# Performance work log

Measured on AMD Instinct MI355X. Metric: run time of the kernel, lower is better.

Reference implementation:

```python
import jax, jax.numpy as jnp
import numpy as np
from jax import lax

CHAR_EMB = 30      # char_embedding_dim
N_FILT = 30        # num_cnn_filter (depthwise multiplier)
KSIZE = 3          # char_kernel_size
WORD_EMB = 100     # word_embedding_dim
MAX_WLEN = 40      # max_word_len
N_CHARS = 102      # characters.id + 2
VOCAB = 400002     # GloVe 400k + unk + pad


def setup_inputs() -> dict:
    key = jax.random.key(0)
    k1, k2, k3, k4, k5, k6 = jax.random.split(key, 6)
    B, S = 64, 128
    char_ids = jax.random.randint(k1, (B, S, MAX_WLEN), 0, N_CHARS)
    word_ids = jax.random.randint(k2, (B, S), 0, VOCAB)
    bound = (3.0 / CHAR_EMB) ** 0.5
    char_emb = jax.random.uniform(k3, (N_CHARS, CHAR_EMB), minval=-bound, maxval=bound, dtype=jnp.float32)
    # grouped Conv1d: out=CHAR_EMB*N_FILT=900, in_per_group=1, kernel=3 (OIH layout)
    fan = 1 * KSIZE + N_FILT * KSIZE
    xav = (6.0 / fan) ** 0.5
    conv_w = jax.random.uniform(k4, (CHAR_EMB * N_FILT, 1, KSIZE), minval=-xav, maxval=xav, dtype=jnp.float32)
    conv_b = jnp.zeros((CHAR_EMB * N_FILT,), dtype=jnp.float32)
    glove = jax.random.normal(k5, (VOCAB, WORD_EMB), dtype=jnp.float32)
    return {"char_ids": char_ids, "word_ids": word_ids, "char_emb": char_emb,
            "conv_w": conv_w, "conv_b": conv_b, "glove": glove}


def reference(char_ids, word_ids, char_emb, conv_w, conv_b, glove):
    B, S, W = char_ids.shape
    # char embedding lookup: [B,S,W,E] -> NCH layout [B*S, E, W]
    x = char_emb[char_ids]                       # [B,S,W,30]
    x = jnp.transpose(x, (0, 1, 3, 2)).reshape(B * S, CHAR_EMB, W)
    # depthwise (grouped) conv, groups=30, multiplier=30 -> 900 out channels, length W-K+1
    y = lax.conv_general_dilated(
        x, conv_w, window_strides=(1,), padding="VALID",
        dimension_numbers=("NCH", "OIH", "NCH"),
        feature_group_count=CHAR_EMB)            # [B*S, 900, 38]
    y = y + conv_b[None, :, None]
    pooled = jnp.max(y, axis=2).reshape(B, S, CHAR_EMB * N_FILT)  # max-over-time
    glove_e = glove[word_ids]                    # [B,S,100]
    return jnp.concatenate([pooled, glove_e], axis=2)  # [B,S,1000]
```

## Files before the change

### kernel.cpp

```cpp
#include <hip/hip_runtime.h>

#define CHAR_EMB 30
#define NFILT    30
#define WLEN     40
#define TOUT     38
#define OUTC     900
#define WORD_EMB 100
#define RP2      42

typedef float f32x2 __attribute__((ext_vector_type(2)));
typedef float f32x4 __attribute__((ext_vector_type(4)));

__device__ __forceinline__ f32x2 pk_fma(f32x2 a, f32x2 b, f32x2 c) {
    f32x2 d;
    asm("v_pk_fma_f32 %0, %1, %2, %3" : "=v"(d) : "v"(a), "v"(b), "v"(c));
    return d;
}
__device__ __forceinline__ f32x2 pk_mul(f32x2 a, f32x2 b) {
    f32x2 d;
    asm("v_pk_mul_f32 %0, %1, %2" : "=v"(d) : "v"(a), "v"(b));
    return d;
}
__device__ __forceinline__ float max3f(float a, float b, float c) {
    float d;
    asm("v_max3_f32 %0, %1, %2, %3" : "=v"(d) : "v"(a), "v"(b), "v"(c));
    return d;
}

__global__ __launch_bounds__(256, 8) void encoder_kernel(
    const int*   __restrict__ char_ids,
    const int*   __restrict__ word_ids,
    const float* __restrict__ char_emb,
    const float* __restrict__ conv_w,
    const float* __restrict__ conv_b,
    const float* __restrict__ glove,
    float*       __restrict__ out,
    int BS)
{
    const int nA   = 2 * blockIdx.x;
    const int nB   = nA + 1;
    const bool hasB = (nB < BS);
    const int tid  = threadIdx.x;

    __shared__ int cid[2 * WLEN];
    __shared__ __align__(16) f32x2 xs[CHAR_EMB * RP2];

    float* orowA = out + (long)nA * (OUTC + WORD_EMB);
    float* orowB = out + (long)nB * (OUTC + WORD_EMB);

    if (tid < 2 * WLEN) {
        cid[tid] = (tid < WLEN || hasB) ? char_ids[nA * WLEN + tid] : 0;
    }
    __syncthreads();

    for (int i = tid; i < WLEN * (CHAR_EMB / 2); i += 256) {
        const int t  = i / (CHAR_EMB / 2);
        const int cp = i - t * (CHAR_EMB / 2);
        const int c  = 2 * cp;
        const f32x2 a = *reinterpret_cast<const f32x2*>(char_emb + cid[t] * CHAR_EMB + c);
        const f32x2 b = *reinterpret_cast<const f32x2*>(char_emb + cid[WLEN + t] * CHAR_EMB + c);
        f32x2 v0; v0.x = a.x; v0.y = b.x;
        f32x2 v1; v1.x = a.y; v1.y = b.y;
        xs[(c    ) * RP2 + t] = v0;
        xs[(c + 1) * RP2 + t] = v1;
    }
    __syncthreads();

    if (tid < 240) {
        const int g = tid >> 3;
        const int j = tid & 7;

        f32x2 W0[4], W1[4], W2[4];
        float bias[4];
        #pragma unroll
        for (int u = 0; u < 4; ++u) {
            const int f = j + 8 * u;
            float w0 = 0.f, w1 = 0.f, w2 = 0.f, bb = 0.f;
            if (f < NFILT) {
                const int o = g * NFILT + f;
                w0 = conv_w[o * 3 + 0];
                w1 = conv_w[o * 3 + 1];
                w2 = conv_w[o * 3 + 2];
                bb = conv_b[o];
            }
            W0[u].x = w0; W0[u].y = w0;
            W1[u].x = w1; W1[u].y = w1;
            W2[u].x = w2; W2[u].y = w2;
            bias[u] = bb;
        }

        f32x2 m[4];
        #pragma unroll
        for (int u = 0; u < 4; ++u) { m[u].x = -3.4e38f; m[u].y = -3.4e38f; }

        const f32x4* rp = reinterpret_cast<const f32x4*>(&xs[g * RP2]);
        f32x4 cur = rp[0];
        #pragma unroll 2
        for (int k = 0; k < 19; ++k) {
            const f32x4 nxt = rp[k + 1];
            const f32x2 x0 = cur.xy;
            const f32x2 x1 = cur.zw;
            const f32x2 x2 = nxt.xy;
            const f32x2 x3 = nxt.zw;
            #pragma unroll
            for (int u = 0; u < 4; ++u) {
                const f32x2 v0 = pk_fma(W0[u], x0, pk_fma(W1[u], x1, pk_mul(W2[u], x2)));
                const f32x2 v1 = pk_fma(W0[u], x1, pk_fma(W1[u], x2, pk_mul(W2[u], x3)));
                m[u].x = max3f(m[u].x, v0.x, v1.x);
                m[u].y = max3f(m[u].y, v0.y, v1.y);
            }
            cur = nxt;
        }

        #pragma unroll
        for (int u = 0; u < 4; ++u) {
            const int f = j + 8 * u;
            if (f < NFILT) {
                const int o = g * NFILT + f;
                const float bb = bias[u];
                orowA[o] = m[u].x + bb;
                if (hasB) orowB[o] = m[u].y + bb;
            }
        }
    } else {
        const int k = tid - 240;
        {
            const f32x4* gp = reinterpret_cast<const f32x4*>(glove + (long)word_ids[nA] * WORD_EMB);
            f32x4* op = reinterpret_cast<f32x4*>(orowA + OUTC);
            #pragma unroll
            for (int q = 0; q < 2; ++q) {
                const int idx = k + 16 * q;
                if (idx < WORD_EMB / 4) op[idx] = gp[idx];
            }
        }
        if (hasB) {
            const f32x4* gp = reinterpret_cast<const f32x4*>(glove + (long)word_ids[nB] * WORD_EMB);
            f32x4* op = reinterpret_cast<f32x4*>(orowB + OUTC);
            #pragma unroll
            for (int q = 0; q < 2; ++q) {
                const int idx = k + 16 * q;
                if (idx < WORD_EMB / 4) op[idx] = gp[idx];
            }
        }
    }
}

extern "C" void kernel_launch(void* const* d_in, const int* in_sizes, int n_in,
                              void* d_out, int out_size, void* d_ws, size_t ws_size,
                              hipStream_t stream) {
    const int*   char_ids = (const int*)  d_in[0];
    const int*   word_ids = (const int*)  d_in[1];
    const float* char_emb = (const float*)d_in[2];
    const float* conv_w   = (const float*)d_in[3];
    const float* conv_b   = (const float*)d_in[4];
    const float* glove    = (const float*)d_in[5];
    float*       out      = (float*)      d_out;

    const int BS = in_sizes[1];
    const int nblk = (BS + 1) / 2;

    encoder_kernel<<<nblk, 256, 0, stream>>>(
        char_ids, word_ids, char_emb, conv_w, conv_b, glove, out, BS);
}
```

Baseline: 228.3 us.

## Process eight words per block with double-buffered char-embedding prefetch

Each block now handles eight words as four pairs instead of a single pair. The char-embedding gather for the next pair is issued into registers before the current pair's convolution and written to a second shared buffer afterwards, so gather latency overlaps compute. Weights are loaded once per block and the glove rows for all eight words are copied by the spare threads up front. This cuts block count and per-block setup cost, but reduces grid parallelism, raises register pressure (launch bounds lowered to 4) and adds barriers between pairs.

Result: slower. 235.7 us (+3.3%).

```diff
diff --git a/kernel.cpp b/kernel.cpp
--- a/kernel.cpp
+++ b/kernel.cpp
@@ -7,6 +7,8 @@
 #define OUTC     900
 #define WORD_EMB 100
 #define RP2      42
+#define WORDS    8
+#define PAIRS    4
 
 typedef float f32x2 __attribute__((ext_vector_type(2)));
 typedef float f32x4 __attribute__((ext_vector_type(4)));
@@ -27,7 +29,24 @@
     return d;
 }
 
-__global__ __launch_bounds__(256, 8) void encoder_kernel(
+__device__ __forceinline__ void gather_pair(const int* __restrict__ cq,
+                                            f32x2* __restrict__ dst,
+                                            const float* __restrict__ char_emb,
+                                            int tid)
+{
+    for (int i = tid; i < WLEN * (CHAR_EMB / 2); i += 240) {
+        const int t = i / 15;
+        const int c = 2 * (i - 15 * t);
+        const f32x2 a = *reinterpret_cast<const f32x2*>(char_emb + cq[t] * CHAR_EMB + c);
+        const f32x2 b = *reinterpret_cast<const f32x2*>(char_emb + cq[WLEN + t] * CHAR_EMB + c);
+        f32x2 v0; v0.x = a.x; v0.y = b.x;
+        f32x2 v1; v1.x = a.y; v1.y = b.y;
+        dst[(c    ) * RP2 + t] = v0;
+        dst[(c + 1) * RP2 + t] = v1;
+    }
+}
+
+__global__ __launch_bounds__(256, 4) void encoder_kernel(
     const int*   __restrict__ char_ids,
     const int*   __restrict__ word_ids,
     const float* __restrict__ char_emb,
@@ -37,41 +56,50 @@
     float*       __restrict__ out,
     int BS)
 {
-    const int nA   = 2 * blockIdx.x;
-    const int nB   = nA + 1;
-    const bool hasB = (nB < BS);
-    const int tid  = threadIdx.x;
-
-    __shared__ int cid[2 * WLEN];
-    __shared__ __align__(16) f32x2 xs[CHAR_EMB * RP2];
-
-    float* orowA = out + (long)nA * (OUTC + WORD_EMB);
-    float* orowB = out + (long)nB * (OUTC + WORD_EMB);
-
-    if (tid < 2 * WLEN) {
-        cid[tid] = (tid < WLEN || hasB) ? char_ids[nA * WLEN + tid] : 0;
+    const int nbase = WORDS * (int)blockIdx.x;
+    const int tid   = threadIdx.x;
+
+    __shared__ int cid[WORDS * WLEN];
+    __shared__ __align__(16) f32x2 xs[2][CHAR_EMB * RP2];
+
+    for (int i = tid; i < WORDS * WLEN; i += 256) {
+        const int w = i / WLEN;
+        cid[i] = (nbase + w < BS) ? char_ids[(long)nbase * WLEN + i] : 0;
     }
     __syncthreads();
 
-    for (int i = tid; i < WLEN * (CHAR_EMB / 2); i += 256) {
-        const int t  = i / (CHAR_EMB / 2);
-        const int cp = i - t * (CHAR_EMB / 2);
-        const int c  = 2 * cp;
-        const f32x2 a = *reinterpret_cast<const f32x2*>(char_emb + cid[t] * CHAR_EMB + c);
-        const f32x2 b = *reinterpret_cast<const f32x2*>(char_emb + cid[WLEN + t] * CHAR_EMB + c);
-        f32x2 v0; v0.x = a.x; v0.y = b.x;
-        f32x2 v1; v1.x = a.y; v1.y = b.y;
-        xs[(c    ) * RP2 + t] = v0;
-        xs[(c + 1) * RP2 + t] = v1;
-    }
-    __syncthreads();
-
     if (tid < 240) {
-        const int g = tid >> 3;
-        const int j = tid & 7;
-
-        f32x2 W0[4], W1[4], W2[4];
-        float bias[4];
+        gather_pair(&cid[0], xs[0], char_emb, tid);
+    } else {
+        const int k = tid - 240;
+        f32x4 gv[13];
+        #pragma unroll
+        for (int s = 0; s < 13; ++s) {
+            const int i = k + 16 * s;
+            if (i < WORDS * 25) {
+                const int w = i / 25, ch = i - 25 * w;
+                if (nbase + w < BS)
+                    gv[s] = reinterpret_cast<const f32x4*>(
+                        glove + (long)word_ids[nbase + w] * WORD_EMB)[ch];
+            }
+        }
+        #pragma unroll
+        for (int s = 0; s < 13; ++s) {
+            const int i = k + 16 * s;
+            if (i < WORDS * 25) {
+                const int w = i / 25, ch = i - 25 * w;
+                if (nbase + w < BS)
+                    reinterpret_cast<f32x4*>(
+                        out + (long)(nbase + w) * (OUTC + WORD_EMB) + OUTC)[ch] = gv[s];
+            }
+        }
+    }
+
+    const int g = tid >> 3;
+    const int j = tid & 7;
+    f32x2 W0[4], W1[4], W2[4];
+    float bias[4];
+    if (tid < 240) {
         #pragma unroll
         for (int u = 0; u < 4; ++u) {
             const int f = j + 8 * u;
@@ -88,59 +116,94 @@
             W2[u].x = w2; W2[u].y = w2;
             bias[u] = bb;
         }
-
-        f32x2 m[4];
-        #pragma unroll
-        for (int u = 0; u < 4; ++u) { m[u].x = -3.4e38f; m[u].y = -3.4e38f; }
-
-        const f32x4* rp = reinterpret_cast<const f32x4*>(&xs[g * RP2]);
-        f32x4 cur = rp[0];
-        #pragma unroll 2
-        for (int k = 0; k < 19; ++k) {
-            const f32x4 nxt = rp[k + 1];
-            const f32x2 x0 = cur.xy;
-            const f32x2 x1 = cur.zw;
-            const f32x2 x2 = nxt.xy;
-            const f32x2 x3 = nxt.zw;
+    }
+    __syncthreads();
+
+    #pragma unroll 1
+    for (int q = 0; q < PAIRS; ++q) {
+        f32x2 pa0, pb0, pa1, pb1, pa2, pb2;
+        int t0 = 0, c0 = 0, t1 = 0, c1 = 0, t2 = 0, c2 = 0;
+        const bool pf = (q < PAIRS - 1) && (tid < 240);
+        if (pf) {
+            const int* cq = &cid[(q + 1) * 2 * WLEN];
+            {
+                const int i = tid;
+                t0 = i / 15; c0 = 2 * (i - 15 * t0);
+                pa0 = *reinterpret_cast<const f32x2*>(char_emb + cq[t0] * CHAR_EMB + c0);
+                pb0 = *reinterpret_cast<const f32x2*>(char_emb + cq[WLEN + t0] * CHAR_EMB + c0);
+            }
+            {
+                const int i = tid + 240;
+                t1 = i / 15; c1 = 2 * (i - 15 * t1);
+                pa1 = *reinterpret_cast<const f32x2*>(char_emb + cq[t1] * CHAR_EMB + c1);
+                pb1 = *reinterpret_cast<const f32x2*>(char_emb + cq[WLEN + t1] * CHAR_EMB + c1);
+            }
+            {
+                const int i = (tid < 120) ? tid + 480 : tid;
+                t2 = i / 15; c2 = 2 * (i - 15 * t2);
+                pa2 = *reinterpret_cast<const f32x2*>(char_emb + cq[t2] * CHAR_EMB + c2);
+                pb2 = *reinterpret_cast<const f32x2*>(char_emb + cq[WLEN + t2] * CHAR_EMB + c2);
+            }
+        }
+
+        if (tid < 240) {
+            f32x2 m[4];
+            #pragma unroll
+            for (int u = 0; u < 4; ++u) { m[u].x = -3.4e38f; m[u].y = -3.4e38f; }
+
+            const f32x4* rp = reinterpret_cast<const f32x4*>(&xs[q & 1][g * RP2]);
+            f32x4 cur = rp[0];
+            #pragma unroll 2
+            for (int k = 0; k < 19; ++k) {
+                const f32x4 nxt = rp[k + 1];
+                const f32x2 x0 = cur.xy;
+                const f32x2 x1 = cur.zw;
+                const f32x2 x2 = nxt.xy;
+                const f32x2 x3 = nxt.zw;
+                #pragma unroll
+                for (int u = 0; u < 4; ++u) {
+                    const f32x2 v0 = pk_fma(W0[u], x0, pk_fma(W1[u], x1, pk_mul(W2[u], x2)));
+                    const f32x2 v1 = pk_fma(W0[u], x1, pk_fma(W1[u], x2, pk_mul(W2[u], x3)));
+                    m[u].x = max3f(m[u].x, v0.x, v1.x);
+                    m[u].y = max3f(m[u].y, v0.y, v1.y);
+                }
+                cur = nxt;
+            }
+
+            const int wA = nbase + 2 * q;
+            const int wB = wA + 1;
+            float* orowA = out + (long)wA * (OUTC + WORD_EMB);
+            float* orowB = out + (long)wB * (OUTC + WORD_EMB);
             #pragma unroll
             for (int u = 0; u < 4; ++u) {
-                const f32x2 v0 = pk_fma(W0[u], x0, pk_fma(W1[u], x1, pk_mul(W2[u], x2)));
-                const f32x2 v1 = pk_fma(W0[u], x1, pk_fma(W1[u], x2, pk_mul(W2[u], x3)));
-                m[u].x = max3f(m[u].x, v0.x, v1.x);
-                m[u].y = max3f(m[u].y, v0.y, v1.y);
-            }
-            cur = nxt;
-        }
-
-        #pragma unroll
-        for (int u = 0; u < 4; ++u) {
-            const int f = j + 8 * u;
-            if (f < NFILT) {
-                const int o = g * NFILT + f;
-                const float bb = bias[u];
-                orowA[o] = m[u].x + bb;
-                if (hasB) orowB[o] = m[u].y + bb;
-            }
-        }
-    } else {
-        const int k = tid - 240;
-        {
-            const f32x4* gp = reinterpret_cast<const f32x4*>(glove + (long)word_ids[nA] * WORD_EMB);
-            f32x4* op = reinterpret_cast<f32x4*>(orowA + OUTC);
-            #pragma unroll
-            for (int q = 0; q < 2; ++q) {
-                const int idx = k + 16 * q;
-                if (idx < WORD_EMB / 4) op[idx] = gp[idx];
-            }
-        }
-        if (hasB) {
-            const f32x4* gp = reinterpret_cast<const f32x4*>(glove + (long)word_ids[nB] * WORD_EMB);
-            f32x4* op = reinterpret_cast<f32x4*>(orowB + OUTC);
-            #pragma unroll
-            for (int q = 0; q < 2; ++q) {
-                const int idx = k + 16 * q;
-                if (idx < WORD_EMB / 4) op[idx] = gp[idx];
-            }
+                const int f = j + 8 * u;
+                if (f < NFILT) {
+                    const int o = g * NFILT + f;
+                    const float bb = bias[u];
+                    if (wA < BS) orowA[o] = m[u].x + bb;
+                    if (wB < BS) orowB[o] = m[u].y + bb;
+                }
+            }
+        }
+
+        if (q < PAIRS - 1) {
+            if (pf) {
+                f32x2* dst = xs[(q + 1) & 1];
+                { f32x2 v0; v0.x = pa0.x; v0.y = pb0.x;
+                  f32x2 v1; v1.x = pa0.y; v1.y = pb0.y;
+                  dst[(c0    ) * RP2 + t0] = v0;
+                  dst[(c0 + 1) * RP2 + t0] = v1; }
+                { f32x2 v0; v0.x = pa1.x; v0.y = pb1.x;
+                  f32x2 v1; v1.x = pa1.y; v1.y = pb1.y;
+                  dst[(c1    ) * RP2 + t1] = v0;
+                  dst[(c1 + 1) * RP2 + t1] = v1; }
+                if (tid < 120) {
+                  f32x2 v0; v0.x = pa2.x; v0.y = pb2.x;
+                  f32x2 v1; v1.x = pa2.y; v1.y = pb2.y;
+                  dst[(c2    ) * RP2 + t2] = v0;
+                  dst[(c2 + 1) * RP2 + t2] = v1; }
+            }
+            __syncthreads();
         }
     }
 }
@@ -157,7 +220,7 @@
     float*       out      = (float*)      d_out;
 
     const int BS = in_sizes[1];
-    const int nblk = (BS + 1) / 2;
+    const int nblk = (BS + WORDS - 1) / WORDS;
 
     encoder_kernel<<<nblk, 256, 0, stream>>>(
         char_ids, word_ids, char_emb, conv_w, conv_b, glove, out, BS);
```
